# Kernel optimization log

Measured on AMD Instinct MI355X. Metric: run time of the kernel, lower is better.

The kernel has to match this reference:

```python
import jax, jax.numpy as jnp
import numpy as np

PARTITIONS = 8
TWO_PI = 2.0 * np.pi
EPS_COUNT = 0.0001  # added to bin counts to avoid div-by-zero


def setup_inputs() -> dict:
    key = jax.random.key(0)
    k1, k2, k3, k4 = jax.random.split(key, 4)
    B, N, T = 16384, 128, 8
    trajs = jax.random.normal(k1, (B, T, 2), dtype=jnp.float32)
    nei_trajs = jax.random.normal(k2, (B, N, T, 2), dtype=jnp.float32)
    # mark last 32 neighbors as invalid (all-zero trajectories -> masked out)
    nei_trajs = nei_trajs.at[:, N - 32:].set(0.0)
    # TrajEncoding: Dense(dim=3 -> output_units=128) + ReLU
    W_ce = jax.random.normal(k3, (3, 128), dtype=jnp.float32) * (1.0 / np.sqrt(3.0))
    b_ce = jnp.zeros((128,), dtype=jnp.float32)
    return {"trajs": trajs, "nei_trajs": nei_trajs, "W_ce": W_ce, "b_ce": b_ce}


def reference(trajs, nei_trajs, W_ce, b_ce):
    # trajs: [B, T, 2]; nei_trajs: [B, N, T, 2]
    nei_vector = nei_trajs[..., -1, :] - nei_trajs[..., 0, :]      # [B, N, 2]
    nei_pos = nei_trajs[..., -1, :]                                 # [B, N, 2]

    # factors (use_velocity, use_distance, use_direction; rel_velocity=False)
    f_velocity = jnp.linalg.norm(nei_vector, axis=-1)               # [B, N]
    f_distance = jnp.linalg.norm(nei_pos, axis=-1)                  # [B, N]
    f_direction = jnp.arctan2(nei_pos[..., 0], nei_pos[..., 1]) % TWO_PI  # [B, N]

    angle_idx = (f_direction / (TWO_PI / PARTITIONS)).astype(jnp.int32)   # [B, N]
    nei_mask = (jnp.sum(nei_trajs, axis=(-1, -2)) != 0).astype(jnp.int32)  # [B, N]
    angle_idx = angle_idx * nei_mask + (-1) * (1 - nei_mask)

    # one-hot over partitions replaces the python loop: [B, N, P]
    onehot = (angle_idx[..., None] == jnp.arange(PARTITIONS, dtype=jnp.int32)).astype(jnp.float32)
    n = jnp.sum(onehot, axis=1) + EPS_COUNT                         # [B, P]

    feats = jnp.stack([f_velocity, f_distance, f_direction], axis=-1)  # [B, N, 3]
    sums = jnp.einsum('bnf,bnp->bpf', feats, onehot)                # [B, P, 3]
    social_circle = sums / n[..., None]                             # [B, P, 3]

    f_sc = jax.nn.relu(social_circle @ W_ce + b_ce)                 # [B, P, 128]
    return f_sc, social_circle
```

## Files before the change

kernel.cpp:

```cpp
#include <hip/hip_runtime.h>
#include <math.h>

#define NPART 8
#define NN    128
#define WPB   4

__global__ __launch_bounds__(256) void sc_kernel(
    const float* __restrict__ nei,
    const float* __restrict__ W,
    const float* __restrict__ bce,
    float* __restrict__ fsc,
    float* __restrict__ scout,
    int Btot)
{
    const int tid  = threadIdx.x;
    const int lane = tid & 63;
    const int wv   = tid >> 6;
    const int b    = blockIdx.x * WPB + wv;
    if (b >= Btot) return;

    __shared__ float s_sum[WPB][NPART * 3];
    __shared__ float s_cnt[WPB][NPART];
    __shared__ float s_sc[WPB][NPART * 3];

    const float4* src = reinterpret_cast<const float4*>(nei) + (size_t)b * (NN * 4);
    float4 a0 = src[lane * 4 + 0];
    float4 c0 = src[lane * 4 + 1];
    float4 d0 = src[lane * 4 + 2];
    float4 e0 = src[lane * 4 + 3];
    float4 a1 = src[256 + lane * 4 + 0];
    float4 c1 = src[256 + lane * 4 + 1];
    float4 d1 = src[256 + lane * 4 + 2];
    float4 e1 = src[256 + lane * 4 + 3];

    const int c0i = 2 * lane, c1i = 2 * lane + 1;
    float2 wr0 = *reinterpret_cast<const float2*>(W + 0 * NN + c0i);
    float2 wr1 = *reinterpret_cast<const float2*>(W + 1 * NN + c0i);
    float2 wr2 = *reinterpret_cast<const float2*>(W + 2 * NN + c0i);
    float2 bb  = *reinterpret_cast<const float2*>(bce + c0i);

    if (lane < NPART * 3) s_sum[wv][lane] = 0.0f;
    if (lane < NPART)     s_cnt[wv][lane] = 0.0f;
    __builtin_amdgcn_wave_barrier();

    const float TWOPI = 6.2831853071795864769f;
    const float STEP  = (float)(6.283185307179586 / 8.0);

    #pragma unroll
    for (int h = 0; h < 2; ++h) {
        float4 a = h ? a1 : a0;
        float4 c = h ? c1 : c0;
        float4 d = h ? d1 : d0;
        float4 e = h ? e1 : e0;

        float total = (((a.x + a.y) + (a.z + a.w)) + ((c.x + c.y) + (c.z + c.w)))
                    + (((d.x + d.y) + (d.z + d.w)) + ((e.x + e.y) + (e.z + e.w)));

        float px = e.z, py = e.w;
        float vx = px - a.x, vy = py - a.y;
        float fvel  = sqrtf(vx * vx + vy * vy);
        float fdist = sqrtf(px * px + py * py);

        float fdir = atan2f(px, py);
        if (fdir < 0.0f) fdir += TWOPI;

        int idx = (int)(fdir / STEP);

        if (total != 0.0f && idx >= 0 && idx < NPART) {
            atomicAdd(&s_sum[wv][idx * 3 + 0], fvel);
            atomicAdd(&s_sum[wv][idx * 3 + 1], fdist);
            atomicAdd(&s_sum[wv][idx * 3 + 2], fdir);
            atomicAdd(&s_cnt[wv][idx], 1.0f);
        }
    }
    __builtin_amdgcn_wave_barrier();

    if (lane < NPART * 3) {
        float v = s_sum[wv][lane] / (s_cnt[wv][lane / 3] + 0.0001f);
        s_sc[wv][lane] = v;
        scout[(size_t)b * (NPART * 3) + lane] = v;
    }
    __builtin_amdgcn_wave_barrier();

    float* o = fsc + (size_t)b * NPART * NN;
    #pragma unroll
    for (int p = 0; p < NPART; ++p) {
        float sv = s_sc[wv][p * 3 + 0];
        float sd = s_sc[wv][p * 3 + 1];
        float sr = s_sc[wv][p * 3 + 2];
        float2 acc;
        acc.x = fmaxf(fmaf(sv, wr0.x, fmaf(sd, wr1.x, fmaf(sr, wr2.x, bb.x))), 0.0f);
        acc.y = fmaxf(fmaf(sv, wr0.y, fmaf(sd, wr1.y, fmaf(sr, wr2.y, bb.y))), 0.0f);
        *reinterpret_cast<float2*>(o + p * NN + c0i) = acc;
    }
}

extern "C" void kernel_launch(void* const* d_in, const int* in_sizes, int n_in,
                              void* d_out, int out_size, void* d_ws, size_t ws_size,
                              hipStream_t stream) {
    const float* nei = (const float*)d_in[1];
    const float* W   = (const float*)d_in[2];
    const float* bce = (const float*)d_in[3];

    const int Btot = in_sizes[1] / (NN * 8 * 2);

    float* fsc   = (float*)d_out;
    float* scout = fsc + (size_t)Btot * NPART * NN;

    const int nblk = (Btot + WPB - 1) / WPB;
    sc_kernel<<<nblk, 256, 0, stream>>>(nei, W, bce, fsc, scout, Btot);
}
```

Before: 43.90 us.

## Process four batch rows per wave with double-buffered register prefetch

Each wavefront now loops over four consecutive batch rows, loading the next row's neighbour trajectories into a second register buffer while the current row is binned and projected. The output projection switches to float4 stores, with half-waves covering alternate partitions. The grid shrinks by four, trading fewer resident waves and higher register use for software-pipelined loads and amortised weight loads.

Result: slower. 52.66 us (+19.9%).

```diff
diff --git a/kernel.cpp b/kernel.cpp
--- a/kernel.cpp
+++ b/kernel.cpp
@@ -4,6 +4,7 @@
 #define NPART 8
 #define NN    128
 #define WPB   4
+#define BPW   4
 
 __global__ __launch_bounds__(256) void sc_kernel(
     const float* __restrict__ nei,
@@ -16,82 +17,100 @@
     const int tid  = threadIdx.x;
     const int lane = tid & 63;
     const int wv   = tid >> 6;
-    const int b    = blockIdx.x * WPB + wv;
-    if (b >= Btot) return;
+    const int base = (blockIdx.x * WPB + wv) * BPW;
 
     __shared__ float s_sum[WPB][NPART * 3];
     __shared__ float s_cnt[WPB][NPART];
     __shared__ float s_sc[WPB][NPART * 3];
 
-    const float4* src = reinterpret_cast<const float4*>(nei) + (size_t)b * (NN * 4);
-    float4 a0 = src[lane * 4 + 0];
-    float4 c0 = src[lane * 4 + 1];
-    float4 d0 = src[lane * 4 + 2];
-    float4 e0 = src[lane * 4 + 3];
-    float4 a1 = src[256 + lane * 4 + 0];
-    float4 c1 = src[256 + lane * 4 + 1];
-    float4 d1 = src[256 + lane * 4 + 2];
-    float4 e1 = src[256 + lane * 4 + 3];
-
-    const int c0i = 2 * lane, c1i = 2 * lane + 1;
-    float2 wr0 = *reinterpret_cast<const float2*>(W + 0 * NN + c0i);
-    float2 wr1 = *reinterpret_cast<const float2*>(W + 1 * NN + c0i);
-    float2 wr2 = *reinterpret_cast<const float2*>(W + 2 * NN + c0i);
-    float2 bb  = *reinterpret_cast<const float2*>(bce + c0i);
-
-    if (lane < NPART * 3) s_sum[wv][lane] = 0.0f;
-    if (lane < NPART)     s_cnt[wv][lane] = 0.0f;
-    __builtin_amdgcn_wave_barrier();
+    const int c0i = 4 * (lane & 31);
+    float4 wr0 = *reinterpret_cast<const float4*>(W + 0 * NN + c0i);
+    float4 wr1 = *reinterpret_cast<const float4*>(W + 1 * NN + c0i);
+    float4 wr2 = *reinterpret_cast<const float4*>(W + 2 * NN + c0i);
+    float4 bb  = *reinterpret_cast<const float4*>(bce + c0i);
 
     const float TWOPI = 6.2831853071795864769f;
     const float STEP  = (float)(6.283185307179586 / 8.0);
 
+    const float4* nei4 = reinterpret_cast<const float4*>(nei);
+
+    float4 buf[2][8];
+
+    if (base < Btot) {
+        const float4* s = nei4 + (size_t)base * (NN * 4);
+        #pragma unroll
+        for (int k = 0; k < 4; ++k) buf[0][k]     = s[lane * 4 + k];
+        #pragma unroll
+        for (int k = 0; k < 4; ++k) buf[0][4 + k] = s[256 + lane * 4 + k];
+    }
+
     #pragma unroll
-    for (int h = 0; h < 2; ++h) {
-        float4 a = h ? a1 : a0;
-        float4 c = h ? c1 : c0;
-        float4 d = h ? d1 : d0;
-        float4 e = h ? e1 : e0;
+    for (int i = 0; i < BPW; ++i) {
+        const int b = base + i;
+        if (b < Btot) {
+            if (i + 1 < BPW && b + 1 < Btot) {
+                const float4* s = nei4 + (size_t)(b + 1) * (NN * 4);
+                #pragma unroll
+                for (int k = 0; k < 4; ++k) buf[(i + 1) & 1][k]     = s[lane * 4 + k];
+                #pragma unroll
+                for (int k = 0; k < 4; ++k) buf[(i + 1) & 1][4 + k] = s[256 + lane * 4 + k];
+            }
 
-        float total = (((a.x + a.y) + (a.z + a.w)) + ((c.x + c.y) + (c.z + c.w)))
-                    + (((d.x + d.y) + (d.z + d.w)) + ((e.x + e.y) + (e.z + e.w)));
+            if (lane < NPART * 3) s_sum[wv][lane] = 0.0f;
+            if (lane < NPART)     s_cnt[wv][lane] = 0.0f;
+            __builtin_amdgcn_wave_barrier();
 
-        float px = e.z, py = e.w;
-        float vx = px - a.x, vy = py - a.y;
-        float fvel  = sqrtf(vx * vx + vy * vy);
-        float fdist = sqrtf(px * px + py * py);
+            #pragma unroll
+            for (int h = 0; h < 2; ++h) {
+                float4 a = buf[i & 1][h * 4 + 0];
+                float4 c = buf[i & 1][h * 4 + 1];
+                float4 d = buf[i & 1][h * 4 + 2];
+                float4 e = buf[i & 1][h * 4 + 3];
 
-        float fdir = atan2f(px, py);
-        if (fdir < 0.0f) fdir += TWOPI;
+                float total = (((a.x + a.y) + (a.z + a.w)) + ((c.x + c.y) + (c.z + c.w)))
+                            + (((d.x + d.y) + (d.z + d.w)) + ((e.x + e.y) + (e.z + e.w)));
 
-        int idx = (int)(fdir / STEP);
+                float px = e.z, py = e.w;
+                float vx = px - a.x, vy = py - a.y;
+                float fvel  = sqrtf(vx * vx + vy * vy);
+                float fdist = sqrtf(px * px + py * py);
 
-        if (total != 0.0f && idx >= 0 && idx < NPART) {
-            atomicAdd(&s_sum[wv][idx * 3 + 0], fvel);
-            atomicAdd(&s_sum[wv][idx * 3 + 1], fdist);
-            atomicAdd(&s_sum[wv][idx * 3 + 2], fdir);
-            atomicAdd(&s_cnt[wv][idx], 1.0f);
+                float fdir = atan2f(px, py);
+                if (fdir < 0.0f) fdir += TWOPI;
+
+                int idx = (int)(fdir / STEP);
+
+                if (total != 0.0f && idx >= 0 && idx < NPART) {
+                    atomicAdd(&s_sum[wv][idx * 3 + 0], fvel);
+                    atomicAdd(&s_sum[wv][idx * 3 + 1], fdist);
+                    atomicAdd(&s_sum[wv][idx * 3 + 2], fdir);
+                    atomicAdd(&s_cnt[wv][idx], 1.0f);
+                }
+            }
+            __builtin_amdgcn_wave_barrier();
+
+            if (lane < NPART * 3) {
+                float v = s_sum[wv][lane] / (s_cnt[wv][lane / 3] + 0.0001f);
+                s_sc[wv][lane] = v;
+                scout[(size_t)b * (NPART * 3) + lane] = v;
+            }
+            __builtin_amdgcn_wave_barrier();
+
+            float* o = fsc + (size_t)b * NPART * NN;
+            #pragma unroll
+            for (int s = 0; s < 4; ++s) {
+                int p = 2 * s + (lane >> 5);
+                float sv = s_sc[wv][p * 3 + 0];
+                float sd = s_sc[wv][p * 3 + 1];
+                float sr = s_sc[wv][p * 3 + 2];
+                float4 acc;
+                acc.x = fmaxf(fmaf(sv, wr0.x, fmaf(sd, wr1.x, fmaf(sr, wr2.x, bb.x))), 0.0f);
+                acc.y = fmaxf(fmaf(sv, wr0.y, fmaf(sd, wr1.y, fmaf(sr, wr2.y, bb.y))), 0.0f);
+                acc.z = fmaxf(fmaf(sv, wr0.z, fmaf(sd, wr1.z, fmaf(sr, wr2.z, bb.z))), 0.0f);
+                acc.w = fmaxf(fmaf(sv, wr0.w, fmaf(sd, wr1.w, fmaf(sr, wr2.w, bb.w))), 0.0f);
+                *reinterpret_cast<float4*>(o + p * NN + c0i) = acc;
+            }
         }
-    }
-    __builtin_amdgcn_wave_barrier();
-
-    if (lane < NPART * 3) {
-        float v = s_sum[wv][lane] / (s_cnt[wv][lane / 3] + 0.0001f);
-        s_sc[wv][lane] = v;
-        scout[(size_t)b * (NPART * 3) + lane] = v;
-    }
-    __builtin_amdgcn_wave_barrier();
-
-    float* o = fsc + (size_t)b * NPART * NN;
-    #pragma unroll
-    for (int p = 0; p < NPART; ++p) {
-        float sv = s_sc[wv][p * 3 + 0];
-        float sd = s_sc[wv][p * 3 + 1];
-        float sr = s_sc[wv][p * 3 + 2];
-        float2 acc;
-        acc.x = fmaxf(fmaf(sv, wr0.x, fmaf(sd, wr1.x, fmaf(sr, wr2.x, bb.x))), 0.0f);
-        acc.y = fmaxf(fmaf(sv, wr0.y, fmaf(sd, wr1.y, fmaf(sr, wr2.y, bb.y))), 0.0f);
-        *reinterpret_cast<float2*>(o + p * NN + c0i) = acc;
     }
 }
 
@@ -107,6 +126,6 @@
     float* fsc   = (float*)d_out;
     float* scout = fsc + (size_t)Btot * NPART * NN;
 
-    const int nblk = (Btot + WPB - 1) / WPB;
+    const int nblk = (Btot + WPB * BPW - 1) / (WPB * BPW);
     sc_kernel<<<nblk, 256, 0, stream>>>(nei, W, bce, fsc, scout, Btot);
 }
```
